# Kernel tuning notes

Measured on AMD Instinct MI355X. Metric: run time of the kernel, lower is better.

## Reference

```python
import jax, jax.numpy as jnp
import numpy as np

ACTIVE_TASK = 0
K = 4  # top-k experts

def setup_inputs() -> dict:
    key = jax.random.key(0)
    k1, k2, k3, k4 = jax.random.split(key, 4)
    B, L, H, E, T = 16, 8192, 768, 16, 8
    x = jax.random.normal(k1, (B, L, H), jnp.float32)
    task_full = jax.random.normal(k2, (T, H), jnp.float32)
    gate_w = jax.random.normal(k3, (H, E), jnp.float32) * 0.02   # f_gate Linear weight (transposed)
    gate_b = jnp.zeros((E,), jnp.float32)                         # f_gate Linear bias
    expert_w = jax.random.normal(k4, (E, H, H), jnp.float32) * 0.02  # ParallelExperts weight [E, in, out]
    return {"x": x, "task_full": task_full, "gate_w": gate_w, "gate_b": gate_b, "expert_w": expert_w}

def reference(x, task_full, gate_w, gate_b, expert_w):
    T = task_full.shape[0]
    E = gate_w.shape[1]
    # f_gate = SiLU -> Linear
    logits = jax.nn.silu(task_full) @ gate_w + gate_b            # [T, E]
    probs = jax.nn.softmax(logits, axis=1)                       # [T, E]
    top_k_gates, top_k_indices = jax.lax.top_k(probs, K)         # [T, K]
    # probs_full_quantized: one-hot mask of selected experts per task
    probs_full_quantized = jnp.zeros((T, E), jnp.float32).at[
        jnp.arange(T)[:, None], top_k_indices].set(1.0)
    active_probs = probs[ACTIVE_TASK]                            # [E]
    gates = top_k_gates[ACTIVE_TASK]                             # [K]
    idx = top_k_indices[ACTIVE_TASK]                             # [K] int
    # compute_gating on a single task row: batch_index = arange(K)//K == 0 for all
    # slots, so every selected expert consumes a copy of x[0] (length rows each),
    # and index_add accumulates all K weighted expert outputs into out[0].
    h = jnp.einsum('ld,kdo->klo', x[0], expert_w[idx])           # grouped expert GEMM [K, L, H]
    out0 = jnp.einsum('k,klo->lo', gates, h)                     # gate-weighted combine [L, H]
    out = jnp.zeros_like(x).at[0].add(out0)                      # scatter-add at batch_index (all 0)
    return 1.0 + out, active_probs, probs_full_quantized
```

## Files before the change

kernel.cpp:

```cpp
#include <hip/hip_runtime.h>
#include <hip/hip_bf16.h>

typedef __attribute__((ext_vector_type(8))) short short8;
typedef __attribute__((ext_vector_type(4))) float f32x4;

#define H_DIM 768
#define E_EXP 16
#define T_TASK 8
#define KSEL 4
#define L_SEQ 8192
#define B_BATCH 16
#define EW_STRIDE (768*768)

#define CVT_BLOCKS 3072
#define WCT_BLOCKS 576
#define FILL1_BLOCKS 1408
#define GEMM_BLOCKS 384
#define FILL2_BLOCKS 1472

__global__ __launch_bounds__(256) void k1_cvt_wct_fill(
    const float4* __restrict__ x,
    const float* __restrict__ task_full,
    const float* __restrict__ gate_w,
    const float* __restrict__ gate_b,
    const float* __restrict__ expert_w,
    __hip_bfloat16* __restrict__ wct,
    uint4* __restrict__ xb,
    float* __restrict__ out_tail,
    float4* __restrict__ fill_p, size_t fill_n4) {
  const int bid = blockIdx.x;
  const int tid = threadIdx.x;
  if (bid < CVT_BLOCKS) {
    const int i = bid * 256 + tid;
    const float4 a = x[2 * i];
    const float4 b = x[2 * i + 1];
    alignas(16) __hip_bfloat16 h[8];
    h[0] = __float2bfloat16(a.x); h[1] = __float2bfloat16(a.y);
    h[2] = __float2bfloat16(a.z); h[3] = __float2bfloat16(a.w);
    h[4] = __float2bfloat16(b.x); h[5] = __float2bfloat16(b.y);
    h[6] = __float2bfloat16(b.z); h[7] = __float2bfloat16(b.w);
    xb[i] = *(const uint4*)h;
  } else if (bid < CVT_BLOCKS + WCT_BLOCKS) {
    __shared__ float silu_s[T_TASK * H_DIM];
    __shared__ float logits[T_TASK][E_EXP];
    __shared__ float g_sh[KSEL];
    __shared__ int   i_sh[KSEL];
    __shared__ float tile[32][33];
    const int wb = bid - CVT_BLOCKS;
    for (int i = tid; i < T_TASK * H_DIM; i += 256) {
      float v = task_full[i];
      silu_s[i] = v / (1.f + expf(-v));
    }
    __syncthreads();
    if (tid < T_TASK * E_EXP) {
      const int t = tid >> 4, e = tid & 15;
      float a0 = 0.f, a1 = 0.f, a2 = 0.f, a3 = 0.f;
      const float* sl = &silu_s[t * H_DIM];
      for (int h = 0; h < H_DIM; h += 4) {
        a0 += sl[h]     * gate_w[(h)     * E_EXP + e];
        a1 += sl[h + 1] * gate_w[(h + 1) * E_EXP + e];
        a2 += sl[h + 2] * gate_w[(h + 2) * E_EXP + e];
        a3 += sl[h + 3] * gate_w[(h + 3) * E_EXP + e];
      }
      logits[t][e] = (a0 + a1) + (a2 + a3) + gate_b[e];
    }
    __syncthreads();
    if (tid < T_TASK) {
      const int t = tid;
      float p[E_EXP];
      float m = -1e30f;
      for (int e = 0; e < E_EXP; ++e) m = fmaxf(m, logits[t][e]);
      float s = 0.f;
      for (int e = 0; e < E_EXP; ++e) { p[e] = expf(logits[t][e] - m); s += p[e]; }
      const float inv = 1.f / s;
      for (int e = 0; e < E_EXP; ++e) p[e] *= inv;
      bool used[E_EXP];
      for (int e = 0; e < E_EXP; ++e) used[e] = false;
      float g[KSEL]; int sel[KSEL];
      for (int k = 0; k < KSEL; ++k) {
        float bv = -1.f; int bi = 0;
        for (int e = 0; e < E_EXP; ++e)
          if (!used[e] && p[e] > bv) { bv = p[e]; bi = e; }
        used[bi] = true; sel[k] = bi; g[k] = bv;
      }
      if (wb == 0) {
        for (int e = 0; e < E_EXP; ++e)
          out_tail[E_EXP + t * E_EXP + e] = used[e] ? 1.f : 0.f;
        if (t == 0)
          for (int e = 0; e < E_EXP; ++e) out_tail[e] = p[e];
      }
      if (t == 0)
        for (int k = 0; k < KSEL; ++k) { g_sh[k] = g[k]; i_sh[k] = sel[k]; }
    }
    __syncthreads();
    const float g0 = g_sh[0], g1 = g_sh[1], g2 = g_sh[2], g3 = g_sh[3];
    const size_t e0 = (size_t)i_sh[0] * EW_STRIDE;
    const size_t e1 = (size_t)i_sh[1] * EW_STRIDE;
    const size_t e2 = (size_t)i_sh[2] * EW_STRIDE;
    const size_t e3 = (size_t)i_sh[3] * EW_STRIDE;
    const int d0 = (wb % 24) * 32, o0 = (wb / 24) * 32;
    const int c = tid & 31;
    const int r0 = tid >> 5;
#pragma unroll
    for (int it = 0; it < 4; ++it) {
      const int rr = it * 8 + r0;
      const size_t off = (size_t)(d0 + rr) * H_DIM + o0 + c;
      tile[rr][c] = g0 * expert_w[e0 + off] + g1 * expert_w[e1 + off] +
                    g2 * expert_w[e2 + off] + g3 * expert_w[e3 + off];
    }
    __syncthreads();
#pragma unroll
    for (int it = 0; it < 4; ++it) {
      const int rr = it * 8 + r0;
      wct[(size_t)(o0 + rr) * H_DIM + d0 + c] = __float2bfloat16(tile[c][rr]);
    }
  } else {
    const int fb = bid - CVT_BLOCKS - WCT_BLOCKS;
    size_t i = (size_t)fb * 256 + tid;
    const size_t stride = (size_t)FILL1_BLOCKS * 256;
    const float4 one = make_float4(1.f, 1.f, 1.f, 1.f);
    for (; i < fill_n4; i += stride) fill_p[i] = one;
  }
}

__device__ __forceinline__ void gload_lds16(const void* g, void* l) {
  __builtin_amdgcn_global_load_lds((const __attribute__((address_space(1))) void*)g,
                                   (__attribute__((address_space(3))) void*)l, 16, 0, 0);
}

__global__ __launch_bounds__(256) void k2_gemm_fill(
    const __hip_bfloat16* __restrict__ A,
    const __hip_bfloat16* __restrict__ Bt,
    float* __restrict__ C,
    float4* __restrict__ fill_p, size_t fill_n4) {
  const int bid = blockIdx.x;
  const int tid = threadIdx.x;
  if (bid < GEMM_BLOCKS) {
    __shared__ __hip_bfloat16 As[128 * 32];
    __shared__ __hip_bfloat16 Bs[128 * 32];
    const int m0 = (bid / 6) * 128;
    const int n0 = (bid % 6) * 128;
    const int lane = tid & 63;
    const int w = tid >> 6;
    const int wr = w >> 1, wc = w & 1;
    const int r = tid >> 2, s = tid & 3;
    const __hip_bfloat16* ga = A  + (size_t)(m0 + r) * H_DIM + s * 8;
    const __hip_bfloat16* gb = Bt + (size_t)(n0 + r) * H_DIM + s * 8;
    f32x4 acc[4][4] = {};
    const int arow = wr * 64 + (lane & 15);
    const int brow = wc * 64 + (lane & 15);
    const int koff = (lane >> 4) * 8;
    for (int k0 = 0; k0 < H_DIM; k0 += 32) {
      gload_lds16(ga + k0,               &As[tid * 8]);
      gload_lds16(ga + 64 * H_DIM + k0,  &As[2048 + tid * 8]);
      gload_lds16(gb + k0,               &Bs[tid * 8]);
      gload_lds16(gb + 64 * H_DIM + k0,  &Bs[2048 + tid * 8]);
      __syncthreads();
      short8 av[4], bv[4];
#pragma unroll
      for (int i = 0; i < 4; ++i) av[i] = *(const short8*)&As[(arow + i * 16) * 32 + koff];
#pragma unroll
      for (int j = 0; j < 4; ++j) bv[j] = *(const short8*)&Bs[(brow + j * 16) * 32 + koff];
#pragma unroll
      for (int i = 0; i < 4; ++i)
#pragma unroll
        for (int j = 0; j < 4; ++j)
          acc[i][j] = __builtin_amdgcn_mfma_f32_16x16x32_bf16(av[i], bv[j], acc[i][j], 0, 0, 0);
      __syncthreads();
    }
    const int crow0 = m0 + wr * 64 + (lane >> 4) * 4;
    const int ccol0 = n0 + wc * 64 + (lane & 15);
#pragma unroll
    for (int i = 0; i < 4; ++i)
#pragma unroll
      for (int j = 0; j < 4; ++j)
#pragma unroll
        for (int q = 0; q < 4; ++q)
          C[(size_t)(crow0 + i * 16 + q) * H_DIM + ccol0 + j * 16] = 1.0f + acc[i][j][q];
  } else {
    const int fb = bid - GEMM_BLOCKS;
    size_t i = (size_t)fb * 256 + tid;
    const size_t stride = (size_t)FILL2_BLOCKS * 256;
    const float4 one = make_float4(1.f, 1.f, 1.f, 1.f);
    for (; i < fill_n4; i += stride) fill_p[i] = one;
  }
}

extern "C" void kernel_launch(void* const* d_in, const int* in_sizes, int n_in,
                              void* d_out, int out_size, void* d_ws, size_t ws_size,
                              hipStream_t stream) {
  const float* x         = (const float*)d_in[0];
  const float* task_full = (const float*)d_in[1];
  const float* gate_w    = (const float*)d_in[2];
  const float* gate_b    = (const float*)d_in[3];
  const float* expert_w  = (const float*)d_in[4];
  float* out = (float*)d_out;

  const size_t n_out_main = (size_t)B_BATCH * L_SEQ * H_DIM;
  float* out_tail = out + n_out_main;

  __hip_bfloat16* wct = (__hip_bfloat16*)d_ws;
  __hip_bfloat16* x0b = (__hip_bfloat16*)((char*)d_ws + (size_t)EW_STRIDE * 2);

  const size_t fill1_n4 = (size_t)8 * L_SEQ * H_DIM / 4;
  k1_cvt_wct_fill<<<CVT_BLOCKS + WCT_BLOCKS + FILL1_BLOCKS, 256, 0, stream>>>(
      (const float4*)x, task_full, gate_w, gate_b, expert_w,
      wct, (uint4*)x0b, out_tail,
      (float4*)(out + (size_t)1 * L_SEQ * H_DIM), fill1_n4);

  const size_t fill2_n4 = (size_t)7 * L_SEQ * H_DIM / 4;
  k2_gemm_fill<<<GEMM_BLOCKS + FILL2_BLOCKS, 256, 0, stream>>>(
      x0b, wct, out,
      (float4*)(out + (size_t)9 * L_SEQ * H_DIM), fill2_n4);
}
```

Baseline: 119.3 us.

## Fuse x fp32-to-bf16 conversion into GEMM with register-staged double buffering

Removes the separate pass that converted x[0] to bf16 in the first kernel; the GEMM now loads fp32 x directly, converts in registers, and writes to a double-buffered LDS with a software pipeline instead of global_load_lds. The GEMM tile shrinks from 128x128 to 64x128 (768 blocks), and the fill work is rebalanced so most of the output fill runs alongside the GEMM. This saves a bf16 round trip through workspace, at the cost of reading fp32 A six times (once per column block) and losing the direct-to-LDS loads.

```diff
diff --git a/kernel.cpp b/kernel.cpp
--- a/kernel.cpp
+++ b/kernel.cpp
@@ -12,41 +12,28 @@
 #define B_BATCH 16
 #define EW_STRIDE (768*768)
 
-#define CVT_BLOCKS 3072
 #define WCT_BLOCKS 576
-#define FILL1_BLOCKS 1408
-#define GEMM_BLOCKS 384
-#define FILL2_BLOCKS 1472
-
-__global__ __launch_bounds__(256) void k1_cvt_wct_fill(
-    const float4* __restrict__ x,
+#define FILL1_BLOCKS 448
+#define GEMM_BLOCKS 768
+#define FILL2_BLOCKS 1280
+
+__global__ __launch_bounds__(256) void k1_wct_fill(
     const float* __restrict__ task_full,
     const float* __restrict__ gate_w,
     const float* __restrict__ gate_b,
     const float* __restrict__ expert_w,
     __hip_bfloat16* __restrict__ wct,
-    uint4* __restrict__ xb,
     float* __restrict__ out_tail,
     float4* __restrict__ fill_p, size_t fill_n4) {
   const int bid = blockIdx.x;
   const int tid = threadIdx.x;
-  if (bid < CVT_BLOCKS) {
-    const int i = bid * 256 + tid;
-    const float4 a = x[2 * i];
-    const float4 b = x[2 * i + 1];
-    alignas(16) __hip_bfloat16 h[8];
-    h[0] = __float2bfloat16(a.x); h[1] = __float2bfloat16(a.y);
-    h[2] = __float2bfloat16(a.z); h[3] = __float2bfloat16(a.w);
-    h[4] = __float2bfloat16(b.x); h[5] = __float2bfloat16(b.y);
-    h[6] = __float2bfloat16(b.z); h[7] = __float2bfloat16(b.w);
-    xb[i] = *(const uint4*)h;
-  } else if (bid < CVT_BLOCKS + WCT_BLOCKS) {
+  if (bid < WCT_BLOCKS) {
     __shared__ float silu_s[T_TASK * H_DIM];
     __shared__ float logits[T_TASK][E_EXP];
     __shared__ float g_sh[KSEL];
     __shared__ int   i_sh[KSEL];
     __shared__ float tile[32][33];
-    const int wb = bid - CVT_BLOCKS;
+    const int wb = bid;
     for (int i = tid; i < T_TASK * H_DIM; i += 256) {
       float v = task_full[i];
       silu_s[i] = v / (1.f + expf(-v));
@@ -115,7 +102,7 @@
       wct[(size_t)(o0 + rr) * H_DIM + d0 + c] = __float2bfloat16(tile[c][rr]);
     }
   } else {
-    const int fb = bid - CVT_BLOCKS - WCT_BLOCKS;
+    const int fb = bid - WCT_BLOCKS;
     size_t i = (size_t)fb * 256 + tid;
     const size_t stride = (size_t)FILL1_BLOCKS * 256;
     const float4 one = make_float4(1.f, 1.f, 1.f, 1.f);
@@ -123,60 +110,83 @@
   }
 }
 
-__device__ __forceinline__ void gload_lds16(const void* g, void* l) {
-  __builtin_amdgcn_global_load_lds((const __attribute__((address_space(1))) void*)g,
-                                   (__attribute__((address_space(3))) void*)l, 16, 0, 0);
-}
+#define LOADA(S, kk) { \
+    const float* ap_ = X + (size_t)(m0 + ra) * H_DIM + (kk) + sa * 8; \
+    S##_a0 = *(const float4*)ap_; S##_a1 = *(const float4*)(ap_ + 4); }
+#define LOADB(S, kk) { \
+    const __hip_bfloat16* bp_ = Bt + (size_t)(n0 + rb) * H_DIM + (kk); \
+    S##_b0 = *(const short8*)(bp_ + sb * 8); \
+    S##_b1 = *(const short8*)(bp_ + 16 + sb * 8); }
+#define WRITEAB(S, buf) { \
+    alignas(16) __hip_bfloat16 hb_[8]; \
+    hb_[0] = __float2bfloat16(S##_a0.x); hb_[1] = __float2bfloat16(S##_a0.y); \
+    hb_[2] = __float2bfloat16(S##_a0.z); hb_[3] = __float2bfloat16(S##_a0.w); \
+    hb_[4] = __float2bfloat16(S##_a1.x); hb_[5] = __float2bfloat16(S##_a1.y); \
+    hb_[6] = __float2bfloat16(S##_a1.z); hb_[7] = __float2bfloat16(S##_a1.w); \
+    *(short8*)&As[buf][ra * 32 + sa * 8] = *(const short8*)hb_; \
+    *(short8*)&Bs[buf][rb * 32 + sb * 8] = S##_b0; \
+    *(short8*)&Bs[buf][rb * 32 + 16 + sb * 8] = S##_b1; }
+#define FRAGS(buf) { \
+    _Pragma("unroll") for (int i = 0; i < 2; ++i) \
+      av[i] = *(const short8*)&As[buf][(arow + i * 16) * 32 + koff]; \
+    _Pragma("unroll") for (int j = 0; j < 4; ++j) \
+      bv[j] = *(const short8*)&Bs[buf][(brow + j * 16) * 32 + koff]; }
+#define MFMAS() { \
+    _Pragma("unroll") for (int i = 0; i < 2; ++i) \
+      _Pragma("unroll") for (int j = 0; j < 4; ++j) \
+        acc[i][j] = __builtin_amdgcn_mfma_f32_16x16x32_bf16(av[i], bv[j], acc[i][j], 0, 0, 0); }
 
 __global__ __launch_bounds__(256) void k2_gemm_fill(
-    const __hip_bfloat16* __restrict__ A,
+    const float* __restrict__ X,
     const __hip_bfloat16* __restrict__ Bt,
-    float* __restrict__ C,
+    float* __restrict__ out,
     float4* __restrict__ fill_p, size_t fill_n4) {
+  __shared__ unsigned short As[2][64 * 32];
+  __shared__ unsigned short Bs[2][128 * 32];
   const int bid = blockIdx.x;
   const int tid = threadIdx.x;
   if (bid < GEMM_BLOCKS) {
-    __shared__ __hip_bfloat16 As[128 * 32];
-    __shared__ __hip_bfloat16 Bs[128 * 32];
-    const int m0 = (bid / 6) * 128;
+    const int m0 = (bid / 6) * 64;
     const int n0 = (bid % 6) * 128;
     const int lane = tid & 63;
     const int w = tid >> 6;
     const int wr = w >> 1, wc = w & 1;
-    const int r = tid >> 2, s = tid & 3;
-    const __hip_bfloat16* ga = A  + (size_t)(m0 + r) * H_DIM + s * 8;
-    const __hip_bfloat16* gb = Bt + (size_t)(n0 + r) * H_DIM + s * 8;
-    f32x4 acc[4][4] = {};
-    const int arow = wr * 64 + (lane & 15);
+    const int ra = tid >> 2, sa = tid & 3;
+    const int rb = tid >> 1, sb = tid & 1;
+    const int arow = wr * 32 + (lane & 15);
     const int brow = wc * 64 + (lane & 15);
     const int koff = (lane >> 4) * 8;
-    for (int k0 = 0; k0 < H_DIM; k0 += 32) {
-      gload_lds16(ga + k0,               &As[tid * 8]);
-      gload_lds16(ga + 64 * H_DIM + k0,  &As[2048 + tid * 8]);
-      gload_lds16(gb + k0,               &Bs[tid * 8]);
-      gload_lds16(gb + 64 * H_DIM + k0,  &Bs[2048 + tid * 8]);
+    f32x4 acc[2][4] = {};
+    float4 S0_a0, S0_a1, S1_a0, S1_a1;
+    short8 S0_b0, S0_b1, S1_b0, S1_b1;
+    short8 av[2], bv[4];
+    LOADA(S0, 0)  LOADB(S0, 0)
+    LOADA(S1, 32) LOADB(S1, 32)
+    WRITEAB(S0, 0)
+#pragma unroll 1
+    for (int t = 0; t < 24; t += 2) {
       __syncthreads();
-      short8 av[4], bv[4];
-#pragma unroll
-      for (int i = 0; i < 4; ++i) av[i] = *(const short8*)&As[(arow + i * 16) * 32 + koff];
-#pragma unroll
-      for (int j = 0; j < 4; ++j) bv[j] = *(const short8*)&Bs[(brow + j * 16) * 32 + koff];
-#pragma unroll
-      for (int i = 0; i < 4; ++i)
-#pragma unroll
-        for (int j = 0; j < 4; ++j)
-          acc[i][j] = __builtin_amdgcn_mfma_f32_16x16x32_bf16(av[i], bv[j], acc[i][j], 0, 0, 0);
+      LOADA(S0, (t + 2) * 32)
+      LOADB(S0, (t + 2) * 32)
+      FRAGS(0)
+      WRITEAB(S1, 1)
+      MFMAS()
       __syncthreads();
-    }
-    const int crow0 = m0 + wr * 64 + (lane >> 4) * 4;
+      LOADA(S1, (t + 3) * 32)
+      LOADB(S1, (t + 3) * 32)
+      FRAGS(1)
+      WRITEAB(S0, 0)
+      MFMAS()
+    }
+    const int crow0 = m0 + wr * 32 + (lane >> 4) * 4;
     const int ccol0 = n0 + wc * 64 + (lane & 15);
 #pragma unroll
-    for (int i = 0; i < 4; ++i)
+    for (int i = 0; i < 2; ++i)
 #pragma unroll
       for (int j = 0; j < 4; ++j)
 #pragma unroll
         for (int q = 0; q < 4; ++q)
-          C[(size_t)(crow0 + i * 16 + q) * H_DIM + ccol0 + j * 16] = 1.0f + acc[i][j][q];
+          out[(size_t)(crow0 + i * 16 + q) * H_DIM + ccol0 + j * 16] = 1.0f + acc[i][j][q];
   } else {
     const int fb = bid - GEMM_BLOCKS;
     size_t i = (size_t)fb * 256 + tid;
@@ -200,16 +210,14 @@
   float* out_tail = out + n_out_main;
 
   __hip_bfloat16* wct = (__hip_bfloat16*)d_ws;
-  __hip_bfloat16* x0b = (__hip_bfloat16*)((char*)d_ws + (size_t)EW_STRIDE * 2);
-
-  const size_t fill1_n4 = (size_t)8 * L_SEQ * H_DIM / 4;
-  k1_cvt_wct_fill<<<CVT_BLOCKS + WCT_BLOCKS + FILL1_BLOCKS, 256, 0, stream>>>(
-      (const float4*)x, task_full, gate_w, gate_b, expert_w,
-      wct, (uint4*)x0b, out_tail,
-      (float4*)(out + (size_t)1 * L_SEQ * H_DIM), fill1_n4);
-
-  const size_t fill2_n4 = (size_t)7 * L_SEQ * H_DIM / 4;
+
+  const size_t fill1_n4 = (size_t)L_SEQ * H_DIM / 4;
+  k1_wct_fill<<<WCT_BLOCKS + FILL1_BLOCKS, 256, 0, stream>>>(
+      task_full, gate_w, gate_b, expert_w, wct, out_tail,
+      (float4*)(out + (size_t)L_SEQ * H_DIM), fill1_n4);
+
+  const size_t fill2_n4 = (size_t)14 * L_SEQ * H_DIM / 4;
   k2_gemm_fill<<<GEMM_BLOCKS + FILL2_BLOCKS, 256, 0, stream>>>(
-      x0b, wct, out,
-      (float4*)(out + (size_t)9 * L_SEQ * H_DIM), fill2_n4);
+      x, wct, out,
+      (float4*)(out + (size_t)2 * L_SEQ * H_DIM), fill2_n4);
 }
```

New measurement: 143.0 us. 19.9% more time.

## Pipeline GEMM with register prefetch and double-buffered LDS on smaller tiles

Applied to the files above, without the earlier changes.

Replaces the direct global-to-LDS loads and the two barriers per k-step with a software pipeline. Global loads are prefetched three k-steps ahead into registers and written into a double-buffered LDS, so each step needs a single barrier. The GEMM tile shrinks from 128x128 to 128x64, doubling the number of GEMM blocks to improve occupancy and overlap with the fill blocks. The prefetch runs past K on the last steps, reading unused data beyond row ends, and uses more registers.

```diff
diff --git a/kernel.cpp b/kernel.cpp
--- a/kernel.cpp
+++ b/kernel.cpp
@@ -15,7 +15,7 @@
 #define CVT_BLOCKS 3072
 #define WCT_BLOCKS 576
 #define FILL1_BLOCKS 1408
-#define GEMM_BLOCKS 384
+#define GEMM_BLOCKS 768
 #define FILL2_BLOCKS 1472
 
 __global__ __launch_bounds__(256) void k1_cvt_wct_fill(
@@ -123,57 +123,79 @@
   }
 }
 
-__device__ __forceinline__ void gload_lds16(const void* g, void* l) {
-  __builtin_amdgcn_global_load_lds((const __attribute__((address_space(1))) void*)g,
-                                   (__attribute__((address_space(3))) void*)l, 16, 0, 0);
-}
+#define LOADA(S, kk) { \
+    const __hip_bfloat16* ap_ = A + (size_t)(m0 + ra) * H_DIM + (kk) + sa; \
+    S##_a0 = *(const short8*)ap_; S##_a1 = *(const short8*)(ap_ + 8); }
+#define LOADB(S, kk) { \
+    S##_b0 = *(const short8*)(Bt + (size_t)(n0 + rb) * H_DIM + (kk) + sb); }
+#define WRITEAB(S, buf) { \
+    *(short8*)&As[buf][ra * 32 + sa]     = S##_a0; \
+    *(short8*)&As[buf][ra * 32 + sa + 8] = S##_a1; \
+    *(short8*)&Bs[buf][rb * 32 + sb]     = S##_b0; }
+#define FRAGS(buf) { \
+    _Pragma("unroll") for (int i = 0; i < 4; ++i) \
+      av[i] = *(const short8*)&As[buf][(arow + i * 16) * 32 + koff]; \
+    _Pragma("unroll") for (int j = 0; j < 2; ++j) \
+      bv[j] = *(const short8*)&Bs[buf][(brow + j * 16) * 32 + koff]; }
+#define MFMAS() { \
+    _Pragma("unroll") for (int i = 0; i < 4; ++i) \
+      _Pragma("unroll") for (int j = 0; j < 2; ++j) \
+        acc[i][j] = __builtin_amdgcn_mfma_f32_16x16x32_bf16(av[i], bv[j], acc[i][j], 0, 0, 0); }
+#define GSTEP(buf, SW, SL, kld) { \
+    FRAGS(buf) \
+    WRITEAB(SW, buf ^ 1) \
+    LOADA(SL, kld) LOADB(SL, kld) \
+    MFMAS() \
+    asm volatile("s_waitcnt lgkmcnt(0)" ::: "memory"); \
+    __builtin_amdgcn_s_barrier(); }
 
 __global__ __launch_bounds__(256) void k2_gemm_fill(
     const __hip_bfloat16* __restrict__ A,
     const __hip_bfloat16* __restrict__ Bt,
     float* __restrict__ C,
     float4* __restrict__ fill_p, size_t fill_n4) {
+  __shared__ __attribute__((aligned(16))) unsigned short As[2][128 * 32];
+  __shared__ __attribute__((aligned(16))) unsigned short Bs[2][64 * 32];
   const int bid = blockIdx.x;
   const int tid = threadIdx.x;
   if (bid < GEMM_BLOCKS) {
-    __shared__ __hip_bfloat16 As[128 * 32];
-    __shared__ __hip_bfloat16 Bs[128 * 32];
-    const int m0 = (bid / 6) * 128;
-    const int n0 = (bid % 6) * 128;
+    const int m0 = (bid / 12) * 128;
+    const int n0 = (bid % 12) * 64;
     const int lane = tid & 63;
     const int w = tid >> 6;
     const int wr = w >> 1, wc = w & 1;
-    const int r = tid >> 2, s = tid & 3;
-    const __hip_bfloat16* ga = A  + (size_t)(m0 + r) * H_DIM + s * 8;
-    const __hip_bfloat16* gb = Bt + (size_t)(n0 + r) * H_DIM + s * 8;
-    f32x4 acc[4][4] = {};
+    const int ra = tid >> 1, sa = (tid & 1) * 16;
+    const int rb = tid >> 2, sb = (tid & 3) * 8;
     const int arow = wr * 64 + (lane & 15);
-    const int brow = wc * 64 + (lane & 15);
+    const int brow = wc * 32 + (lane & 15);
     const int koff = (lane >> 4) * 8;
-    for (int k0 = 0; k0 < H_DIM; k0 += 32) {
-      gload_lds16(ga + k0,               &As[tid * 8]);
-      gload_lds16(ga + 64 * H_DIM + k0,  &As[2048 + tid * 8]);
-      gload_lds16(gb + k0,               &Bs[tid * 8]);
-      gload_lds16(gb + 64 * H_DIM + k0,  &Bs[2048 + tid * 8]);
-      __syncthreads();
-      short8 av[4], bv[4];
-#pragma unroll
-      for (int i = 0; i < 4; ++i) av[i] = *(const short8*)&As[(arow + i * 16) * 32 + koff];
-#pragma unroll
-      for (int j = 0; j < 4; ++j) bv[j] = *(const short8*)&Bs[(brow + j * 16) * 32 + koff];
-#pragma unroll
-      for (int i = 0; i < 4; ++i)
-#pragma unroll
-        for (int j = 0; j < 4; ++j)
-          acc[i][j] = __builtin_amdgcn_mfma_f32_16x16x32_bf16(av[i], bv[j], acc[i][j], 0, 0, 0);
-      __syncthreads();
+    f32x4 acc[4][2] = {};
+    short8 S0_a0, S0_a1, S0_b0;
+    short8 S1_a0, S1_a1, S1_b0;
+    short8 S2_a0, S2_a1, S2_b0;
+    short8 av[4], bv[2];
+    LOADA(S0, 0)  LOADB(S0, 0)
+    LOADA(S1, 32) LOADB(S1, 32)
+    LOADA(S2, 64) LOADB(S2, 64)
+    WRITEAB(S0, 0)
+    asm volatile("s_waitcnt lgkmcnt(0)" ::: "memory");
+    __builtin_amdgcn_s_barrier();
+#pragma unroll 1
+    for (int t0 = 0; t0 < 24; t0 += 6) {
+      const int kb = t0 * 32;
+      GSTEP(0, S1, S0, kb + 3 * 32)
+      GSTEP(1, S2, S1, kb + 4 * 32)
+      GSTEP(0, S0, S2, kb + 5 * 32)
+      GSTEP(1, S1, S0, kb + 6 * 32)
+      GSTEP(0, S2, S1, kb + 7 * 32)
+      GSTEP(1, S0, S2, kb + 8 * 32)
     }
     const int crow0 = m0 + wr * 64 + (lane >> 4) * 4;
-    const int ccol0 = n0 + wc * 64 + (lane & 15);
+    const int ccol0 = n0 + wc * 32 + (lane & 15);
 #pragma unroll
     for (int i = 0; i < 4; ++i)
 #pragma unroll
-      for (int j = 0; j < 4; ++j)
+      for (int j = 0; j < 2; ++j)
 #pragma unroll
         for (int q = 0; q < 4; ++q)
           C[(size_t)(crow0 + i * 16 + q) * H_DIM + ccol0 + j * 16] = 1.0f + acc[i][j][q];
@@ -206,7 +228,7 @@
   k1_cvt_wct_fill<<<CVT_BLOCKS + WCT_BLOCKS + FILL1_BLOCKS, 256, 0, stream>>>(
       (const float4*)x, task_full, gate_w, gate_b, expert_w,
       wct, (uint4*)x0b, out_tail,
-      (float4*)(out + (size_t)1 * L_SEQ * H_DIM), fill1_n4);
+      (float4*)(out + (size_t)L_SEQ * H_DIM), fill1_n4);
 
   const size_t fill2_n4 = (size_t)7 * L_SEQ * H_DIM / 4;
   k2_gemm_fill<<<GEMM_BLOCKS + FILL2_BLOCKS, 256, 0, stream>>>(
```

Result: slower. 126.4 us (+6.0%).

## Replace LDS-staged 128x128 GEMM tiles with direct-load 64x64 register tiles

Applied to the files above, without the earlier changes.

The GEMM part of the second kernel drops LDS staging and barriers. Each wave now loads its A and B fragments straight from global memory into registers and computes a 16x64 strip, so each block covers a 64x64 tile and the grid grows from 384 to 1536 GEMM blocks. This removes the per-K-step synchronisation and LDS traffic and spreads the work over more blocks. The cost is less data reuse, since each B fragment is reloaded per wave and the global loads are strided 16-byte reads, which rely on cache to keep memory traffic down.

```diff
diff --git a/kernel.cpp b/kernel.cpp
--- a/kernel.cpp
+++ b/kernel.cpp
@@ -15,7 +15,7 @@
 #define CVT_BLOCKS 3072
 #define WCT_BLOCKS 576
 #define FILL1_BLOCKS 1408
-#define GEMM_BLOCKS 384
+#define GEMM_BLOCKS 1536
 #define FILL2_BLOCKS 1472
 
 __global__ __launch_bounds__(256) void k1_cvt_wct_fill(
@@ -123,11 +123,6 @@
   }
 }
 
-__device__ __forceinline__ void gload_lds16(const void* g, void* l) {
-  __builtin_amdgcn_global_load_lds((const __attribute__((address_space(1))) void*)g,
-                                   (__attribute__((address_space(3))) void*)l, 16, 0, 0);
-}
-
 __global__ __launch_bounds__(256) void k2_gemm_fill(
     const __hip_bfloat16* __restrict__ A,
     const __hip_bfloat16* __restrict__ Bt,
@@ -136,47 +131,39 @@
   const int bid = blockIdx.x;
   const int tid = threadIdx.x;
   if (bid < GEMM_BLOCKS) {
-    __shared__ __hip_bfloat16 As[128 * 32];
-    __shared__ __hip_bfloat16 Bs[128 * 32];
-    const int m0 = (bid / 6) * 128;
-    const int n0 = (bid % 6) * 128;
-    const int lane = tid & 63;
-    const int w = tid >> 6;
-    const int wr = w >> 1, wc = w & 1;
-    const int r = tid >> 2, s = tid & 3;
-    const __hip_bfloat16* ga = A  + (size_t)(m0 + r) * H_DIM + s * 8;
-    const __hip_bfloat16* gb = Bt + (size_t)(n0 + r) * H_DIM + s * 8;
-    f32x4 acc[4][4] = {};
-    const int arow = wr * 64 + (lane & 15);
-    const int brow = wc * 64 + (lane & 15);
+    const int m0 = (bid / 12) * 64;
+    const int n0 = (bid % 12) * 64;
+    const int wave = tid >> 6, lane = tid & 63;
+    const int row16 = lane & 15;
     const int koff = (lane >> 4) * 8;
+    const __hip_bfloat16* ap  = A  + (size_t)(m0 + wave * 16 + row16) * H_DIM + koff;
+    const __hip_bfloat16* bp0 = Bt + (size_t)(n0 + row16) * H_DIM + koff;
+    const __hip_bfloat16* bp1 = bp0 + (size_t)16 * H_DIM;
+    const __hip_bfloat16* bp2 = bp0 + (size_t)32 * H_DIM;
+    const __hip_bfloat16* bp3 = bp0 + (size_t)48 * H_DIM;
+    f32x4 acc0 = {}, acc1 = {}, acc2 = {}, acc3 = {};
+#pragma unroll 4
     for (int k0 = 0; k0 < H_DIM; k0 += 32) {
-      gload_lds16(ga + k0,               &As[tid * 8]);
-      gload_lds16(ga + 64 * H_DIM + k0,  &As[2048 + tid * 8]);
-      gload_lds16(gb + k0,               &Bs[tid * 8]);
-      gload_lds16(gb + 64 * H_DIM + k0,  &Bs[2048 + tid * 8]);
-      __syncthreads();
-      short8 av[4], bv[4];
+      const short8 av = *(const short8*)(ap + k0);
+      const short8 b0 = *(const short8*)(bp0 + k0);
+      const short8 b1 = *(const short8*)(bp1 + k0);
+      const short8 b2 = *(const short8*)(bp2 + k0);
+      const short8 b3 = *(const short8*)(bp3 + k0);
+      acc0 = __builtin_amdgcn_mfma_f32_16x16x32_bf16(av, b0, acc0, 0, 0, 0);
+      acc1 = __builtin_amdgcn_mfma_f32_16x16x32_bf16(av, b1, acc1, 0, 0, 0);
+      acc2 = __builtin_amdgcn_mfma_f32_16x16x32_bf16(av, b2, acc2, 0, 0, 0);
+      acc3 = __builtin_amdgcn_mfma_f32_16x16x32_bf16(av, b3, acc3, 0, 0, 0);
+    }
+    const int crow0 = m0 + wave * 16 + (lane >> 4) * 4;
+    const int ccol0 = n0 + row16;
+    float* cp = C + (size_t)crow0 * H_DIM + ccol0;
 #pragma unroll
-      for (int i = 0; i < 4; ++i) av[i] = *(const short8*)&As[(arow + i * 16) * 32 + koff];
-#pragma unroll
-      for (int j = 0; j < 4; ++j) bv[j] = *(const short8*)&Bs[(brow + j * 16) * 32 + koff];
-#pragma unroll
-      for (int i = 0; i < 4; ++i)
-#pragma unroll
-        for (int j = 0; j < 4; ++j)
-          acc[i][j] = __builtin_amdgcn_mfma_f32_16x16x32_bf16(av[i], bv[j], acc[i][j], 0, 0, 0);
-      __syncthreads();
-    }
-    const int crow0 = m0 + wr * 64 + (lane >> 4) * 4;
-    const int ccol0 = n0 + wc * 64 + (lane & 15);
-#pragma unroll
-    for (int i = 0; i < 4; ++i)
-#pragma unroll
-      for (int j = 0; j < 4; ++j)
-#pragma unroll
-        for (int q = 0; q < 4; ++q)
-          C[(size_t)(crow0 + i * 16 + q) * H_DIM + ccol0 + j * 16] = 1.0f + acc[i][j][q];
+    for (int q = 0; q < 4; ++q) {
+      cp[(size_t)q * H_DIM]      = 1.0f + acc0[q];
+      cp[(size_t)q * H_DIM + 16] = 1.0f + acc1[q];
+      cp[(size_t)q * H_DIM + 32] = 1.0f + acc2[q];
+      cp[(size_t)q * H_DIM + 48] = 1.0f + acc3[q];
+    }
   } else {
     const int fb = bid - GEMM_BLOCKS;
     size_t i = (size_t)fb * 256 + tid;
@@ -206,7 +193,7 @@
   k1_cvt_wct_fill<<<CVT_BLOCKS + WCT_BLOCKS + FILL1_BLOCKS, 256, 0, stream>>>(
       (const float4*)x, task_full, gate_w, gate_b, expert_w,
       wct, (uint4*)x0b, out_tail,
-      (float4*)(out + (size_t)1 * L_SEQ * H_DIM), fill1_n4);
+      (float4*)(out + (size_t)L_SEQ * H_DIM), fill1_n4);
 
   const size_t fill2_n4 = (size_t)7 * L_SEQ * H_DIM / 4;
   k2_gemm_fill<<<GEMM_BLOCKS + FILL2_BLOCKS, 256, 0, stream>>>(
```

Result: slower. 178.8 us (+49.9%).
